# Kernel optimization log

Hardware: AMD Instinct MI355X
Metric: run time of the kernel (lower is better)

Reference implementation:

```python
import jax, jax.numpy as jnp
import numpy as np

NUM_HEAD = 16
EMB_DIM = 1024
HEAD_DIM = EMB_DIM // NUM_HEAD

def setup_inputs() -> dict:
    key = jax.random.key(0)
    ks = jax.random.split(key, 9)
    B, S, D = 2, 2048, EMB_DIM
    s = 1.0 / np.sqrt(D)
    return {
        "x": jax.random.normal(ks[0], (B, S, D), dtype=jnp.float32),
        "Wq": jax.random.normal(ks[1], (D, D), dtype=jnp.float32) * s,
        "bq": jnp.zeros((D,), dtype=jnp.float32),
        "Wk": jax.random.normal(ks[2], (D, D), dtype=jnp.float32) * s,
        "bk": jnp.zeros((D,), dtype=jnp.float32),
        "Wv": jax.random.normal(ks[3], (D, D), dtype=jnp.float32) * s,
        "bv": jnp.zeros((D,), dtype=jnp.float32),
        "Wo": jax.random.normal(ks[4], (D, D), dtype=jnp.float32) * s,
        "bo": jnp.zeros((D,), dtype=jnp.float32),
    }

def reference(x, Wq, bq, Wk, bk, Wv, bv, Wo, bo):
    B, S, D = x.shape
    H, Hd = NUM_HEAD, HEAD_DIM
    # projections (torch Linear: x @ W.T + b; here W stored as [in, out])
    Q = (x @ Wq + bq).reshape(B, S, H, Hd)
    K = (x @ Wk + bk).reshape(B, S, H, Hd)
    V = (x @ Wv + bv).reshape(B, S, H, Hd)
    scale = jnp.sqrt(jnp.asarray(Hd, dtype=x.dtype))
    scores = jnp.einsum('bqhd,bkhd->bhqk', Q, K) / scale  # [B,H,S,S]
    attn = jax.nn.softmax(scores, axis=-1)
    out = jnp.einsum('bhql,blhd->bqhd', attn, V).reshape(B, S, D)
    return out @ Wo + bo
```

## Files before the change

kernel.cpp:

```cpp
#include <hip/hip_runtime.h>
#include <math.h>


using bf16   = __bf16;
using bf16x8 = __attribute__((ext_vector_type(8))) __bf16;
using bf16x4 = __attribute__((ext_vector_type(4))) __bf16;
using f32x4  = __attribute__((ext_vector_type(4))) float;

#define MFMA16(a, b, c) __builtin_amdgcn_mfma_f32_16x16x32_bf16((a), (b), (c), 0, 0, 0)
#define WAIT_VM0() asm volatile("s_waitcnt vmcnt(0)" ::: "memory")

__device__ __forceinline__ bf16x8 ld8(const bf16* p) { return *(const bf16x8*)p; }

__device__ __forceinline__ void ldg_lds16(bf16* lds_base, const bf16* g) {
    __builtin_amdgcn_global_load_lds(
        (const __attribute__((address_space(1))) void*)g,
        (__attribute__((address_space(3))) void*)lds_base, 16, 0, 0);
}

__device__ __forceinline__ float fast_exp2(float x) {
#if __has_builtin(__builtin_amdgcn_exp2f)
    return __builtin_amdgcn_exp2f(x);
#else
    return exp2f(x);
#endif
}

__device__ __forceinline__ float rowsum16(float v) {
    v += __shfl_xor(v, 1, 64);
    v += __shfl_xor(v, 2, 64);
    v += __shfl_xor(v, 4, 64);
    v += __shfl_xor(v, 8, 64);
    return v;
}

__global__ __launch_bounds__(256) void convert_x_kernel(const float* __restrict__ x,
                                                        bf16* __restrict__ xb) {
    int i = (blockIdx.x * 256 + threadIdx.x) * 4;
    float4 v = *(const float4*)&x[i];
    bf16x4 o = { (bf16)v.x, (bf16)v.y, (bf16)v.z, (bf16)v.w };
    *(bf16x4*)&xb[i] = o;
}

__global__ __launch_bounds__(256) void transpose_w_kernel(
    const float* __restrict__ Wq, const float* __restrict__ Wk,
    const float* __restrict__ Wv, const float* __restrict__ Wo,
    bf16* __restrict__ WtBase) {
    __shared__ float tile[32][33];
    const int z = blockIdx.z;
    const float* W = (z == 0) ? Wq : (z == 1) ? Wk : (z == 2) ? Wv : Wo;
    bf16* Wt = WtBase + (size_t)z * 1024 * 1024;
    const int tx = threadIdx.x, ty = threadIdx.y;
    const int x0 = blockIdx.x * 32, y0 = blockIdx.y * 32;
#pragma unroll
    for (int i = 0; i < 4; ++i)
        tile[ty + i * 8][tx] = W[(size_t)(y0 + ty + i * 8) * 1024 + x0 + tx];
    __syncthreads();
#pragma unroll
    for (int i = 0; i < 4; ++i)
        Wt[(size_t)(x0 + ty + i * 8) * 1024 + y0 + tx] = (bf16)tile[tx][ty + i * 8];
}

__device__ __forceinline__ void gemm_stage(const bf16* __restrict__ src, int r0,
                                           int k0, bf16* dst, int w, int lane) {
#pragma unroll
    for (int c = 0; c < 2; ++c) {
        int flat = (w * 2 + c) * 64 + lane;
        int row = flat >> 2, cc = flat & 3;
        int gk = (cc ^ ((row >> 1) & 3)) * 8;
        ldg_lds16(dst + (size_t)(w * 2 + c) * 512,
                  src + (size_t)(r0 + row) * 1024 + k0 + gk);
    }
}

__device__ __forceinline__ void gemm_core_128(const bf16* __restrict__ A,
                                              const bf16* __restrict__ Bt,
                                              int m0, int n0,
                                              bf16* As, bf16* Bs,
                                              f32x4 (&acc)[4][4]) {
    const int tid = threadIdx.x, lane = tid & 63, w = tid >> 6;
    const int lo = lane & 15, quad = lane >> 4;
    const int wm = w >> 1, wn = w & 1;

    gemm_stage(A,  m0, 0, As, w, lane);
    gemm_stage(Bt, n0, 0, Bs, w, lane);
    WAIT_VM0();
    __syncthreads();

    for (int it = 0; it < 32; ++it) {
        const int buf = it & 1;
        if (it + 1 < 32) {
            gemm_stage(A,  m0, (it + 1) * 32, As + (buf ^ 1) * 4096, w, lane);
            gemm_stage(Bt, n0, (it + 1) * 32, Bs + (buf ^ 1) * 4096, w, lane);
        }
        const bf16* Ab = As + buf * 4096;
        const bf16* Bb = Bs + buf * 4096;
        bf16x8 af[4], bq[4];
#pragma unroll
        for (int t = 0; t < 4; ++t) {
            int r = wm * 64 + t * 16 + lo;
            af[t] = ld8(&Ab[r * 32 + ((quad ^ ((r >> 1) & 3)) * 8)]);
        }
#pragma unroll
        for (int t = 0; t < 4; ++t) {
            int r = wn * 64 + t * 16 + lo;
            bq[t] = ld8(&Bb[r * 32 + ((quad ^ ((r >> 1) & 3)) * 8)]);
        }
#pragma unroll
        for (int mt = 0; mt < 4; ++mt)
#pragma unroll
            for (int nt = 0; nt < 4; ++nt)
                acc[mt][nt] = MFMA16(af[mt], bq[nt], acc[mt][nt]);
        WAIT_VM0();
        __syncthreads();
    }
}

__global__ __launch_bounds__(256, 3) void qkv_gemm_kernel(
    const bf16* __restrict__ Xb, const bf16* __restrict__ Wts,
    const float* __restrict__ bq, const float* __restrict__ bk,
    const float* __restrict__ bv,
    bf16* __restrict__ Qo, bf16* __restrict__ Ko, bf16* __restrict__ Vto) {
    __shared__ bf16 Smem[4 * 4096];
    bf16* As = Smem;
    bf16* Bs = Smem + 2 * 4096;
    const int z = blockIdx.z;
    const bf16*  Bt   = Wts + (size_t)z * 1024 * 1024;
    const float* bias = (z == 0) ? bq : (z == 1) ? bk : bv;
    const int m0 = blockIdx.y * 128, n0 = blockIdx.x * 128;

    f32x4 acc[4][4] = {};
    gemm_core_128(Xb, Bt, m0, n0, As, Bs, acc);

    const int tid = threadIdx.x;
    const int lane = tid & 63, w = tid >> 6;
    const int lo = lane & 15, quad = lane >> 4;
    const int wm = w >> 1, wn = w & 1;
    const float QSCALE = 0.125f * 1.44269504088896f;

    if (z == 2) {
        bf16* T = Smem;
        const int b = m0 >> 11;
        const int s_base = m0 & 2047;
#pragma unroll
        for (int half = 0; half < 2; ++half) {
            __syncthreads();
            if (wm == half) {
#pragma unroll
                for (int nt = 0; nt < 4; ++nt)
#pragma unroll
                    for (int mt = 0; mt < 4; ++mt)
#pragma unroll
                        for (int r = 0; r < 4; ++r) {
                            int nn = wn * 64 + nt * 16 + lo;
                            int mm = mt * 16 + quad * 4 + r;
                            T[nn * 68 + mm] = (bf16)(acc[mt][nt][r] + bias[n0 + nn]);
                        }
            }
            __syncthreads();
#pragma unroll
            for (int p = 0; p < 8; ++p) {
                int pos = p * 1024 + tid * 4;
                int row = pos >> 6, col = pos & 63;
                int n = n0 + row, h = n >> 6, hd = n & 63;
                bf16x4 v = *(const bf16x4*)&T[row * 68 + col];
                *(bf16x4*)&Vto[((size_t)((b * 16 + h) * 64 + hd) << 11)
                               + s_base + half * 64 + col] = v;
            }
        }
    } else {
#pragma unroll
        for (int mt = 0; mt < 4; ++mt)
#pragma unroll
            for (int nt = 0; nt < 4; ++nt)
#pragma unroll
                for (int r = 0; r < 4; ++r) {
                    int m = m0 + wm * 64 + mt * 16 + quad * 4 + r;
                    int n = n0 + wn * 64 + nt * 16 + lo;
                    float v = acc[mt][nt][r] + bias[n];
                    int b = m >> 11, s = m & 2047, h = n >> 6, hd = n & 63;
                    if (z == 0)
                        Qo[((size_t)((b * 16 + h) * 2048 + s) << 6) + hd] = (bf16)(v * QSCALE);
                    else
                        Ko[((size_t)((b * 16 + h) * 2048 + s) << 6) + hd] = (bf16)v;
                }
    }
}

__global__ __launch_bounds__(256, 2) void out_gemm_kernel(
    const bf16* __restrict__ A, const bf16* __restrict__ Bt,
    const float* __restrict__ bo, float* __restrict__ Co) {
    __shared__ bf16 As[2 * 2048];
    __shared__ bf16 Bs[2 * 4096];
    const int tid = threadIdx.x, lane = tid & 63, w = tid >> 6;
    const int lo = lane & 15, quad = lane >> 4;
    const int wm = w >> 1, wn = w & 1;
    const int m0 = blockIdx.y * 64, n0 = blockIdx.x * 128;

    auto stageA = [&](int k0, bf16* dst) {
        int flat = w * 64 + lane;
        int row = flat >> 2, cc = flat & 3;
        int gk = (cc ^ ((row >> 1) & 3)) * 8;
        ldg_lds16(dst + (size_t)w * 512, A + (size_t)(m0 + row) * 1024 + k0 + gk);
    };
    auto stageB = [&](int k0, bf16* dst) {
#pragma unroll
        for (int c = 0; c < 2; ++c) {
            int flat = (w * 2 + c) * 64 + lane;
            int row = flat >> 2, cc = flat & 3;
            int gk = (cc ^ ((row >> 1) & 3)) * 8;
            ldg_lds16(dst + (size_t)(w * 2 + c) * 512,
                      Bt + (size_t)(n0 + row) * 1024 + k0 + gk);
        }
    };

    f32x4 acc[2][4] = {};
    stageA(0, As);
    stageB(0, Bs);
    WAIT_VM0();
    __syncthreads();

    for (int it = 0; it < 32; ++it) {
        const int buf = it & 1;
        if (it + 1 < 32) {
            stageA((it + 1) * 32, As + (buf ^ 1) * 2048);
            stageB((it + 1) * 32, Bs + (buf ^ 1) * 4096);
        }
        const bf16* Ab = As + buf * 2048;
        const bf16* Bb = Bs + buf * 4096;
        bf16x8 af[2], bq[4];
#pragma unroll
        for (int t = 0; t < 2; ++t) {
            int r = wm * 32 + t * 16 + lo;
            af[t] = ld8(&Ab[r * 32 + ((quad ^ ((r >> 1) & 3)) * 8)]);
        }
#pragma unroll
        for (int t = 0; t < 4; ++t) {
            int r = wn * 64 + t * 16 + lo;
            bq[t] = ld8(&Bb[r * 32 + ((quad ^ ((r >> 1) & 3)) * 8)]);
        }
#pragma unroll
        for (int mt = 0; mt < 2; ++mt)
#pragma unroll
            for (int nt = 0; nt < 4; ++nt)
                acc[mt][nt] = MFMA16(af[mt], bq[nt], acc[mt][nt]);
        WAIT_VM0();
        __syncthreads();
    }

#pragma unroll
    for (int mt = 0; mt < 2; ++mt)
#pragma unroll
        for (int nt = 0; nt < 4; ++nt)
#pragma unroll
            for (int r = 0; r < 4; ++r) {
                int m = m0 + wm * 32 + mt * 16 + quad * 4 + r;
                int n = n0 + wn * 64 + nt * 16 + lo;
                Co[(size_t)m * 1024 + n] = acc[mt][nt][r] + bo[n];
            }
}

#define PSTRIDE 72

__global__ __launch_bounds__(256, 2) void attn_kernel(
    const bf16* __restrict__ Q, const bf16* __restrict__ K,
    const bf16* __restrict__ Vt, bf16* __restrict__ AO) {
    __shared__ bf16 Ks[2][64 * 64];
    __shared__ bf16 Vs[2][64 * 64];
    __shared__ bf16 Pl[4][32 * PSTRIDE];
    const int tid = threadIdx.x, w = tid >> 6, lane = tid & 63;
    const int lo = lane & 15, quad = lane >> 4;
    const int blk = blockIdx.x;
    const int bh = (blk & 7) | ((blk >> 7) << 3);
    const int qb = (blk >> 3) & 15;
    const int q0 = qb * 128 + w * 32;

    const bf16* Qb = Q + ((size_t)bh * 2048 + q0) * 64;
    const bf16* Kb = K + (size_t)bh * 2048 * 64;
    const bf16* Vb = Vt + (size_t)bh * 64 * 2048;
    bf16* Pw = &Pl[w][0];

    bf16x8 qa[2][2];
#pragma unroll
    for (int mt = 0; mt < 2; ++mt)
#pragma unroll
        for (int ks = 0; ks < 2; ++ks)
            qa[mt][ks] = ld8(&Qb[(mt * 16 + lo) * 64 + ks * 32 + quad * 8]);

    f32x4 O[2][4] = {};
    f32x4 l_acc[2] = {};

    auto stage = [&](int s0, int buf) {
#pragma unroll
        for (int c = 0; c < 2; ++c) {
            int flat = (w * 2 + c) * 64 + lane;
            int row = flat >> 3, cc = flat & 7;
            int gK = (cc ^ ((row >> 2) & 7)) * 8;
            int gV = (cc ^ (row & 7)) * 8;
            ldg_lds16(&Ks[buf][(w * 2 + c) * 512], &Kb[(size_t)(s0 + row) * 64 + gK]);
            ldg_lds16(&Vs[buf][(w * 2 + c) * 512], &Vb[(size_t)row * 2048 + s0 + gV]);
        }
    };

    stage(0, 0);
    WAIT_VM0();
    __syncthreads();

    for (int it = 0; it < 32; ++it) {
        const int buf = it & 1;
        if (it + 1 < 32) stage((it + 1) * 64, buf ^ 1);
        const bf16* Kt = &Ks[buf][0];
        const bf16* Vl = &Vs[buf][0];

        f32x4 S[2][4] = {};
#pragma unroll
        for (int t = 0; t < 4; ++t) {
            int r = lo * 4 + t;
#pragma unroll
            for (int ks = 0; ks < 2; ++ks) {
                bf16x8 kf = ld8(&Kt[r * 64 + (((quad + 4 * ks) ^ ((r >> 2) & 7)) * 8)]);
                S[0][t] = MFMA16(qa[0][ks], kf, S[0][t]);
                S[1][t] = MFMA16(qa[1][ks], kf, S[1][t]);
            }
        }
#pragma unroll
        for (int mt = 0; mt < 2; ++mt)
#pragma unroll
            for (int r = 0; r < 4; ++r) {
                float p0 = fast_exp2(S[mt][0][r]);
                float p1 = fast_exp2(S[mt][1][r]);
                float p2 = fast_exp2(S[mt][2][r]);
                float p3 = fast_exp2(S[mt][3][r]);
                l_acc[mt][r] += (p0 + p1) + (p2 + p3);
                bf16x4 pk = { (bf16)p0, (bf16)p1, (bf16)p2, (bf16)p3 };
                *(bf16x4*)&Pw[(mt * 16 + quad * 4 + r) * PSTRIDE + lo * 4] = pk;
            }
#pragma unroll
        for (int mt = 0; mt < 2; ++mt) {
            bf16x8 pa0 = ld8(&Pw[(mt * 16 + lo) * PSTRIDE + quad * 8]);
            bf16x8 pa1 = ld8(&Pw[(mt * 16 + lo) * PSTRIDE + 32 + quad * 8]);
#pragma unroll
            for (int nt = 0; nt < 4; ++nt) {
                int r = nt * 16 + lo;
                bf16x8 v0 = ld8(&Vl[r * 64 + ((quad ^ (r & 7)) * 8)]);
                bf16x8 v1 = ld8(&Vl[r * 64 + (((quad + 4) ^ (r & 7)) * 8)]);
                O[mt][nt] = MFMA16(pa0, v0, O[mt][nt]);
                O[mt][nt] = MFMA16(pa1, v1, O[mt][nt]);
            }
        }
        WAIT_VM0();
        __syncthreads();
    }

    const int bb = bh >> 4, h = bh & 15;
#pragma unroll
    for (int mt = 0; mt < 2; ++mt) {
        const size_t outbase = ((size_t)(bb * 2048 + q0 + mt * 16)) * 1024 + h * 64;
#pragma unroll
        for (int r = 0; r < 4; ++r) {
            float rl = 1.0f / rowsum16(l_acc[mt][r]);
            size_t rowoff = outbase + (size_t)(quad * 4 + r) * 1024;
#pragma unroll
            for (int nt = 0; nt < 4; ++nt)
                AO[rowoff + nt * 16 + lo] = (bf16)(O[mt][nt][r] * rl);
        }
    }
}

extern "C" void kernel_launch(void* const* d_in, const int* in_sizes, int n_in,
                              void* d_out, int out_size, void* d_ws, size_t ws_size,
                              hipStream_t stream) {
    const float* x  = (const float*)d_in[0];
    const float* Wq = (const float*)d_in[1];
    const float* bq = (const float*)d_in[2];
    const float* Wk = (const float*)d_in[3];
    const float* bk = (const float*)d_in[4];
    const float* Wv = (const float*)d_in[5];
    const float* bv = (const float*)d_in[6];
    const float* Wo = (const float*)d_in[7];
    const float* bo = (const float*)d_in[8];
    float* out = (float*)d_out;

    bf16* wsb = (bf16*)d_ws;
    const size_t M1 = 1024u * 1024u;
    bf16* Xb  = wsb;
    bf16* AO  = wsb;
    bf16* Wt  = wsb + 4 * M1;
    bf16* Qw  = wsb + 8 * M1;
    bf16* Kw  = wsb + 12 * M1;
    bf16* Vtw = wsb + 16 * M1;

    convert_x_kernel<<<4096, 256, 0, stream>>>(x, Xb);
    transpose_w_kernel<<<dim3(32, 32, 4), dim3(32, 8), 0, stream>>>(Wq, Wk, Wv, Wo, Wt);
    qkv_gemm_kernel<<<dim3(8, 32, 3), 256, 0, stream>>>(Xb, Wt, bq, bk, bv, Qw, Kw, Vtw);
    attn_kernel<<<512, 256, 0, stream>>>(Qw, Kw, Vtw, AO);
    out_gemm_kernel<<<dim3(8, 64), 256, 0, stream>>>(AO, Wt + 3 * M1, bo, out);
}
```

Baseline: 191.1 us.

## Deepen attention KV pipeline to 4-stage 32-key tiles and merge prep kernels

The attention kernel now streams K/V in 32-key tiles through a 4-deep LDS ring, issuing loads three tiles ahead. It waits with partial vmcnt counts plus a bare barrier instead of draining all loads every iteration, so global-to-LDS copies overlap compute. The x conversion and weight transpose kernels are merged into one launch to save a kernel launch. The trade-off is twice as many loop iterations and barriers, smaller MFMA batches per iteration, and hand-tuned wait counts that must exactly match the number of outstanding loads.

```diff
diff --git a/kernel.cpp b/kernel.cpp
--- a/kernel.cpp
+++ b/kernel.cpp
@@ -5,10 +5,12 @@
 using bf16   = __bf16;
 using bf16x8 = __attribute__((ext_vector_type(8))) __bf16;
 using bf16x4 = __attribute__((ext_vector_type(4))) __bf16;
+using bf16x2 = __attribute__((ext_vector_type(2))) __bf16;
 using f32x4  = __attribute__((ext_vector_type(4))) float;
 
 #define MFMA16(a, b, c) __builtin_amdgcn_mfma_f32_16x16x32_bf16((a), (b), (c), 0, 0, 0)
 #define WAIT_VM0() asm volatile("s_waitcnt vmcnt(0)" ::: "memory")
+#define WAITBAR(N) asm volatile("s_waitcnt vmcnt(" #N ")\n\ts_barrier" ::: "memory")
 
 __device__ __forceinline__ bf16x8 ld8(const bf16* p) { return *(const bf16x8*)p; }
 
@@ -34,23 +36,28 @@
     return v;
 }
 
-__global__ __launch_bounds__(256) void convert_x_kernel(const float* __restrict__ x,
-                                                        bf16* __restrict__ xb) {
-    int i = (blockIdx.x * 256 + threadIdx.x) * 4;
-    float4 v = *(const float4*)&x[i];
-    bf16x4 o = { (bf16)v.x, (bf16)v.y, (bf16)v.z, (bf16)v.w };
-    *(bf16x4*)&xb[i] = o;
-}
-
-__global__ __launch_bounds__(256) void transpose_w_kernel(
-    const float* __restrict__ Wq, const float* __restrict__ Wk,
-    const float* __restrict__ Wv, const float* __restrict__ Wo,
+__global__ __launch_bounds__(256) void prep_kernel(
+    const float* __restrict__ x, const float* __restrict__ Wq,
+    const float* __restrict__ Wk, const float* __restrict__ Wv,
+    const float* __restrict__ Wo, bf16* __restrict__ xb,
     bf16* __restrict__ WtBase) {
+    const int z = blockIdx.z;
+    const int tid = threadIdx.x;
+    if (z == 4) {
+        int id = blockIdx.y * 32 + blockIdx.x;
+#pragma unroll
+        for (int k = 0; k < 4; ++k) {
+            int i = id * 4096 + k * 1024 + tid * 4;
+            float4 v = *(const float4*)&x[i];
+            bf16x4 o = { (bf16)v.x, (bf16)v.y, (bf16)v.z, (bf16)v.w };
+            *(bf16x4*)&xb[i] = o;
+        }
+        return;
+    }
     __shared__ float tile[32][33];
-    const int z = blockIdx.z;
     const float* W = (z == 0) ? Wq : (z == 1) ? Wk : (z == 2) ? Wv : Wo;
     bf16* Wt = WtBase + (size_t)z * 1024 * 1024;
-    const int tx = threadIdx.x, ty = threadIdx.y;
+    const int tx = tid & 31, ty = tid >> 5;
     const int x0 = blockIdx.x * 32, y0 = blockIdx.y * 32;
 #pragma unroll
     for (int i = 0; i < 4; ++i)
@@ -260,14 +267,14 @@
             }
 }
 
-#define PSTRIDE 72
+#define PSTR 36
 
 __global__ __launch_bounds__(256, 2) void attn_kernel(
     const bf16* __restrict__ Q, const bf16* __restrict__ K,
     const bf16* __restrict__ Vt, bf16* __restrict__ AO) {
-    __shared__ bf16 Ks[2][64 * 64];
-    __shared__ bf16 Vs[2][64 * 64];
-    __shared__ bf16 Pl[4][32 * PSTRIDE];
+    __shared__ bf16 Ks[4][32 * 64];
+    __shared__ bf16 Vs[4][64 * 32];
+    __shared__ bf16 Pl[4][32 * PSTR];
     const int tid = threadIdx.x, w = tid >> 6, lane = tid & 63;
     const int lo = lane & 15, quad = lane >> 4;
     const int blk = blockIdx.x;
@@ -290,35 +297,34 @@
     f32x4 O[2][4] = {};
     f32x4 l_acc[2] = {};
 
+    const int kRow = (w * 64 + lane) >> 3, kCc = lane & 7;
+    const int vRow = (w * 64 + lane) >> 2, vCc = lane & 3;
+    const int gKo = (kCc ^ ((kRow >> 2) & 7)) * 8;
+    const int gVo = (vCc ^ (vRow & 3)) * 8;
     auto stage = [&](int s0, int buf) {
-#pragma unroll
-        for (int c = 0; c < 2; ++c) {
-            int flat = (w * 2 + c) * 64 + lane;
-            int row = flat >> 3, cc = flat & 7;
-            int gK = (cc ^ ((row >> 2) & 7)) * 8;
-            int gV = (cc ^ (row & 7)) * 8;
-            ldg_lds16(&Ks[buf][(w * 2 + c) * 512], &Kb[(size_t)(s0 + row) * 64 + gK]);
-            ldg_lds16(&Vs[buf][(w * 2 + c) * 512], &Vb[(size_t)row * 2048 + s0 + gV]);
-        }
+        ldg_lds16(&Ks[buf][w * 512], &Kb[(size_t)(s0 + kRow) * 64 + gKo]);
+        ldg_lds16(&Vs[buf][w * 512], &Vb[(size_t)vRow * 2048 + s0 + gVo]);
     };
 
     stage(0, 0);
-    WAIT_VM0();
-    __syncthreads();
-
-    for (int it = 0; it < 32; ++it) {
-        const int buf = it & 1;
-        if (it + 1 < 32) stage((it + 1) * 64, buf ^ 1);
+    stage(32, 1);
+    stage(64, 2);
+    WAITBAR(4);
+
+    for (int it = 0; it < 64; ++it) {
+        const int buf = it & 3;
+        if (it + 3 < 64) stage((it + 3) * 32, (it + 3) & 3);
         const bf16* Kt = &Ks[buf][0];
         const bf16* Vl = &Vs[buf][0];
 
-        f32x4 S[2][4] = {};
-#pragma unroll
-        for (int t = 0; t < 4; ++t) {
-            int r = lo * 4 + t;
+        f32x4 S[2][2] = {};
+#pragma unroll
+        for (int t = 0; t < 2; ++t) {
+            int r = lo * 2 + t;
+            int sw = (r >> 2) & 7;
 #pragma unroll
             for (int ks = 0; ks < 2; ++ks) {
-                bf16x8 kf = ld8(&Kt[r * 64 + (((quad + 4 * ks) ^ ((r >> 2) & 7)) * 8)]);
+                bf16x8 kf = ld8(&Kt[r * 64 + (((quad + 4 * ks) ^ sw) * 8)]);
                 S[0][t] = MFMA16(qa[0][ks], kf, S[0][t]);
                 S[1][t] = MFMA16(qa[1][ks], kf, S[1][t]);
             }
@@ -329,27 +335,26 @@
             for (int r = 0; r < 4; ++r) {
                 float p0 = fast_exp2(S[mt][0][r]);
                 float p1 = fast_exp2(S[mt][1][r]);
-                float p2 = fast_exp2(S[mt][2][r]);
-                float p3 = fast_exp2(S[mt][3][r]);
-                l_acc[mt][r] += (p0 + p1) + (p2 + p3);
-                bf16x4 pk = { (bf16)p0, (bf16)p1, (bf16)p2, (bf16)p3 };
-                *(bf16x4*)&Pw[(mt * 16 + quad * 4 + r) * PSTRIDE + lo * 4] = pk;
+                l_acc[mt][r] += p0 + p1;
+                bf16x2 pk = { (bf16)p0, (bf16)p1 };
+                *(bf16x2*)&Pw[(mt * 16 + quad * 4 + r) * PSTR + lo * 2] = pk;
             }
+        bf16x8 vf[4];
+#pragma unroll
+        for (int nt = 0; nt < 4; ++nt) {
+            int r = nt * 16 + lo;
+            vf[nt] = ld8(&Vl[r * 32 + ((quad ^ (r & 3)) * 8)]);
+        }
 #pragma unroll
         for (int mt = 0; mt < 2; ++mt) {
-            bf16x8 pa0 = ld8(&Pw[(mt * 16 + lo) * PSTRIDE + quad * 8]);
-            bf16x8 pa1 = ld8(&Pw[(mt * 16 + lo) * PSTRIDE + 32 + quad * 8]);
-#pragma unroll
-            for (int nt = 0; nt < 4; ++nt) {
-                int r = nt * 16 + lo;
-                bf16x8 v0 = ld8(&Vl[r * 64 + ((quad ^ (r & 7)) * 8)]);
-                bf16x8 v1 = ld8(&Vl[r * 64 + (((quad + 4) ^ (r & 7)) * 8)]);
-                O[mt][nt] = MFMA16(pa0, v0, O[mt][nt]);
-                O[mt][nt] = MFMA16(pa1, v1, O[mt][nt]);
-            }
-        }
-        WAIT_VM0();
-        __syncthreads();
+            bf16x8 pa = ld8(&Pw[(mt * 16 + lo) * PSTR + quad * 8]);
+#pragma unroll
+            for (int nt = 0; nt < 4; ++nt)
+                O[mt][nt] = MFMA16(pa, vf[nt], O[mt][nt]);
+        }
+        if (it < 61)       WAITBAR(4);
+        else if (it == 61) WAITBAR(2);
+        else if (it == 62) WAITBAR(0);
     }
 
     const int bb = bh >> 4, h = bh & 15;
@@ -390,8 +395,7 @@
     bf16* Kw  = wsb + 12 * M1;
     bf16* Vtw = wsb + 16 * M1;
 
-    convert_x_kernel<<<4096, 256, 0, stream>>>(x, Xb);
-    transpose_w_kernel<<<dim3(32, 32, 4), dim3(32, 8), 0, stream>>>(Wq, Wk, Wv, Wo, Wt);
+    prep_kernel<<<dim3(32, 32, 5), 256, 0, stream>>>(x, Wq, Wk, Wv, Wo, Xb, Wt);
     qkv_gemm_kernel<<<dim3(8, 32, 3), 256, 0, stream>>>(Xb, Wt, bq, bk, bv, Qw, Kw, Vtw);
     attn_kernel<<<512, 256, 0, stream>>>(Qw, Kw, Vtw, AO);
     out_gemm_kernel<<<dim3(8, 64), 256, 0, stream>>>(AO, Wt + 3 * M1, bo, out);
```

Result: slower. 213.2 us (+11.5%).

## Triple-buffer LDS pipelines in GEMMs and attention; fuse prep kernels

Applied to the files above, without the earlier changes.

Switches the QKV GEMM, output GEMM and attention K/V staging from double to triple buffering. Loads run two tiles ahead, and the wait keeps the newest tile's loads in flight (vmcnt(N)) with a single barrier per iteration instead of a full drain. The x conversion and weight transposes are merged into one prep launch to cut launch overhead. LDS use per block grows, which may lower occupancy, notably for the qkv GEMM declared with 3 blocks per CU.

```diff
diff --git a/kernel.cpp b/kernel.cpp
--- a/kernel.cpp
+++ b/kernel.cpp
@@ -8,7 +8,7 @@
 using f32x4  = __attribute__((ext_vector_type(4))) float;
 
 #define MFMA16(a, b, c) __builtin_amdgcn_mfma_f32_16x16x32_bf16((a), (b), (c), 0, 0, 0)
-#define WAIT_VM0() asm volatile("s_waitcnt vmcnt(0)" ::: "memory")
+#define WAITBAR(N) asm volatile("s_waitcnt vmcnt(" #N ")\n\ts_barrier" ::: "memory")
 
 __device__ __forceinline__ bf16x8 ld8(const bf16* p) { return *(const bf16x8*)p; }
 
@@ -34,23 +34,28 @@
     return v;
 }
 
-__global__ __launch_bounds__(256) void convert_x_kernel(const float* __restrict__ x,
-                                                        bf16* __restrict__ xb) {
-    int i = (blockIdx.x * 256 + threadIdx.x) * 4;
-    float4 v = *(const float4*)&x[i];
-    bf16x4 o = { (bf16)v.x, (bf16)v.y, (bf16)v.z, (bf16)v.w };
-    *(bf16x4*)&xb[i] = o;
-}
-
-__global__ __launch_bounds__(256) void transpose_w_kernel(
-    const float* __restrict__ Wq, const float* __restrict__ Wk,
-    const float* __restrict__ Wv, const float* __restrict__ Wo,
+__global__ __launch_bounds__(256) void prep_kernel(
+    const float* __restrict__ x, const float* __restrict__ Wq,
+    const float* __restrict__ Wk, const float* __restrict__ Wv,
+    const float* __restrict__ Wo, bf16* __restrict__ xb,
     bf16* __restrict__ WtBase) {
+    const int z = blockIdx.z;
+    const int tid = threadIdx.x;
+    if (z == 4) {
+        int id = blockIdx.y * 32 + blockIdx.x;
+#pragma unroll
+        for (int k = 0; k < 4; ++k) {
+            int i = id * 4096 + k * 1024 + tid * 4;
+            float4 v = *(const float4*)&x[i];
+            bf16x4 o = { (bf16)v.x, (bf16)v.y, (bf16)v.z, (bf16)v.w };
+            *(bf16x4*)&xb[i] = o;
+        }
+        return;
+    }
     __shared__ float tile[32][33];
-    const int z = blockIdx.z;
     const float* W = (z == 0) ? Wq : (z == 1) ? Wk : (z == 2) ? Wv : Wo;
     bf16* Wt = WtBase + (size_t)z * 1024 * 1024;
-    const int tx = threadIdx.x, ty = threadIdx.y;
+    const int tx = tid & 31, ty = tid >> 5;
     const int x0 = blockIdx.x * 32, y0 = blockIdx.y * 32;
 #pragma unroll
     for (int i = 0; i < 4; ++i)
@@ -82,19 +87,9 @@
     const int lo = lane & 15, quad = lane >> 4;
     const int wm = w >> 1, wn = w & 1;
 
-    gemm_stage(A,  m0, 0, As, w, lane);
-    gemm_stage(Bt, n0, 0, Bs, w, lane);
-    WAIT_VM0();
-    __syncthreads();
-
-    for (int it = 0; it < 32; ++it) {
-        const int buf = it & 1;
-        if (it + 1 < 32) {
-            gemm_stage(A,  m0, (it + 1) * 32, As + (buf ^ 1) * 4096, w, lane);
-            gemm_stage(Bt, n0, (it + 1) * 32, Bs + (buf ^ 1) * 4096, w, lane);
-        }
-        const bf16* Ab = As + buf * 4096;
-        const bf16* Bb = Bs + buf * 4096;
+    auto body = [&](int rbuf) {
+        const bf16* Ab = As + rbuf * 4096;
+        const bf16* Bb = Bs + rbuf * 4096;
         bf16x8 af[4], bq[4];
 #pragma unroll
         for (int t = 0; t < 4; ++t) {
@@ -111,9 +106,27 @@
 #pragma unroll
             for (int nt = 0; nt < 4; ++nt)
                 acc[mt][nt] = MFMA16(af[mt], bq[nt], acc[mt][nt]);
-        WAIT_VM0();
-        __syncthreads();
-    }
+    };
+
+    gemm_stage(A,  m0, 0,  As, w, lane);
+    gemm_stage(Bt, n0, 0,  Bs, w, lane);
+    gemm_stage(A,  m0, 32, As + 4096, w, lane);
+    gemm_stage(Bt, n0, 32, Bs + 4096, w, lane);
+    WAITBAR(4);
+
+    int rbuf = 0, sbuf = 2;
+    for (int it = 0; it < 30; ++it) {
+        gemm_stage(A,  m0, (it + 2) * 32, As + sbuf * 4096, w, lane);
+        gemm_stage(Bt, n0, (it + 2) * 32, Bs + sbuf * 4096, w, lane);
+        sbuf = (sbuf == 2) ? 0 : sbuf + 1;
+        body(rbuf);
+        WAITBAR(4);
+        rbuf = (rbuf == 2) ? 0 : rbuf + 1;
+    }
+    body(rbuf);
+    WAITBAR(0);
+    rbuf = (rbuf == 2) ? 0 : rbuf + 1;
+    body(rbuf);
 }
 
 __global__ __launch_bounds__(256, 3) void qkv_gemm_kernel(
@@ -121,9 +134,9 @@
     const float* __restrict__ bq, const float* __restrict__ bk,
     const float* __restrict__ bv,
     bf16* __restrict__ Qo, bf16* __restrict__ Ko, bf16* __restrict__ Vto) {
-    __shared__ bf16 Smem[4 * 4096];
+    __shared__ bf16 Smem[6 * 4096];
     bf16* As = Smem;
-    bf16* Bs = Smem + 2 * 4096;
+    bf16* Bs = Smem + 3 * 4096;
     const int z = blockIdx.z;
     const bf16*  Bt   = Wts + (size_t)z * 1024 * 1024;
     const float* bias = (z == 0) ? bq : (z == 1) ? bk : bv;
@@ -190,44 +203,35 @@
 __global__ __launch_bounds__(256, 2) void out_gemm_kernel(
     const bf16* __restrict__ A, const bf16* __restrict__ Bt,
     const float* __restrict__ bo, float* __restrict__ Co) {
-    __shared__ bf16 As[2 * 2048];
-    __shared__ bf16 Bs[2 * 4096];
+    __shared__ bf16 As[3 * 2048];
+    __shared__ bf16 Bs[3 * 4096];
     const int tid = threadIdx.x, lane = tid & 63, w = tid >> 6;
     const int lo = lane & 15, quad = lane >> 4;
     const int wm = w >> 1, wn = w & 1;
     const int m0 = blockIdx.y * 64, n0 = blockIdx.x * 128;
 
-    auto stageA = [&](int k0, bf16* dst) {
-        int flat = w * 64 + lane;
-        int row = flat >> 2, cc = flat & 3;
-        int gk = (cc ^ ((row >> 1) & 3)) * 8;
-        ldg_lds16(dst + (size_t)w * 512, A + (size_t)(m0 + row) * 1024 + k0 + gk);
-    };
-    auto stageB = [&](int k0, bf16* dst) {
+    auto stage = [&](int k0, int buf) {
+        {
+            int flat = w * 64 + lane;
+            int row = flat >> 2, cc = flat & 3;
+            int gk = (cc ^ ((row >> 1) & 3)) * 8;
+            ldg_lds16(As + buf * 2048 + (size_t)w * 512,
+                      A + (size_t)(m0 + row) * 1024 + k0 + gk);
+        }
 #pragma unroll
         for (int c = 0; c < 2; ++c) {
             int flat = (w * 2 + c) * 64 + lane;
             int row = flat >> 2, cc = flat & 3;
             int gk = (cc ^ ((row >> 1) & 3)) * 8;
-            ldg_lds16(dst + (size_t)(w * 2 + c) * 512,
+            ldg_lds16(Bs + buf * 4096 + (size_t)(w * 2 + c) * 512,
                       Bt + (size_t)(n0 + row) * 1024 + k0 + gk);
         }
     };
 
     f32x4 acc[2][4] = {};
-    stageA(0, As);
-    stageB(0, Bs);
-    WAIT_VM0();
-    __syncthreads();
-
-    for (int it = 0; it < 32; ++it) {
-        const int buf = it & 1;
-        if (it + 1 < 32) {
-            stageA((it + 1) * 32, As + (buf ^ 1) * 2048);
-            stageB((it + 1) * 32, Bs + (buf ^ 1) * 4096);
-        }
-        const bf16* Ab = As + buf * 2048;
-        const bf16* Bb = Bs + buf * 4096;
+    auto body = [&](int rbuf) {
+        const bf16* Ab = As + rbuf * 2048;
+        const bf16* Bb = Bs + rbuf * 4096;
         bf16x8 af[2], bq[4];
 #pragma unroll
         for (int t = 0; t < 2; ++t) {
@@ -244,9 +248,24 @@
 #pragma unroll
             for (int nt = 0; nt < 4; ++nt)
                 acc[mt][nt] = MFMA16(af[mt], bq[nt], acc[mt][nt]);
-        WAIT_VM0();
-        __syncthreads();
-    }
+    };
+
+    stage(0, 0);
+    stage(32, 1);
+    WAITBAR(3);
+
+    int rbuf = 0, sbuf = 2;
+    for (int it = 0; it < 30; ++it) {
+        stage((it + 2) * 32, sbuf);
+        sbuf = (sbuf == 2) ? 0 : sbuf + 1;
+        body(rbuf);
+        WAITBAR(3);
+        rbuf = (rbuf == 2) ? 0 : rbuf + 1;
+    }
+    body(rbuf);
+    WAITBAR(0);
+    rbuf = (rbuf == 2) ? 0 : rbuf + 1;
+    body(rbuf);
 
 #pragma unroll
     for (int mt = 0; mt < 2; ++mt)
@@ -265,8 +284,8 @@
 __global__ __launch_bounds__(256, 2) void attn_kernel(
     const bf16* __restrict__ Q, const bf16* __restrict__ K,
     const bf16* __restrict__ Vt, bf16* __restrict__ AO) {
-    __shared__ bf16 Ks[2][64 * 64];
-    __shared__ bf16 Vs[2][64 * 64];
+    __shared__ bf16 Ks[3][64 * 64];
+    __shared__ bf16 Vs[3][64 * 64];
     __shared__ bf16 Pl[4][32 * PSTRIDE];
     const int tid = threadIdx.x, w = tid >> 6, lane = tid & 63;
     const int lo = lane & 15, quad = lane >> 4;
@@ -302,16 +321,9 @@
         }
     };
 
-    stage(0, 0);
-    WAIT_VM0();
-    __syncthreads();
-
-    for (int it = 0; it < 32; ++it) {
-        const int buf = it & 1;
-        if (it + 1 < 32) stage((it + 1) * 64, buf ^ 1);
-        const bf16* Kt = &Ks[buf][0];
-        const bf16* Vl = &Vs[buf][0];
-
+    auto body = [&](int rbuf) {
+        const bf16* Kt = &Ks[rbuf][0];
+        const bf16* Vl = &Vs[rbuf][0];
         f32x4 S[2][4] = {};
 #pragma unroll
         for (int t = 0; t < 4; ++t) {
@@ -348,9 +360,24 @@
                 O[mt][nt] = MFMA16(pa1, v1, O[mt][nt]);
             }
         }
-        WAIT_VM0();
-        __syncthreads();
-    }
+    };
+
+    stage(0, 0);
+    stage(64, 1);
+    WAITBAR(4);
+
+    int rbuf = 0, sbuf = 2;
+    for (int it = 0; it < 30; ++it) {
+        stage((it + 2) * 64, sbuf);
+        sbuf = (sbuf == 2) ? 0 : sbuf + 1;
+        body(rbuf);
+        WAITBAR(4);
+        rbuf = (rbuf == 2) ? 0 : rbuf + 1;
+    }
+    body(rbuf);
+    WAITBAR(0);
+    rbuf = (rbuf == 2) ? 0 : rbuf + 1;
+    body(rbuf);
 
     const int bb = bh >> 4, h = bh & 15;
 #pragma unroll
@@ -390,8 +417,7 @@
     bf16* Kw  = wsb + 12 * M1;
     bf16* Vtw = wsb + 16 * M1;
 
-    convert_x_kernel<<<4096, 256, 0, stream>>>(x, Xb);
-    transpose_w_kernel<<<dim3(32, 32, 4), dim3(32, 8), 0, stream>>>(Wq, Wk, Wv, Wo, Wt);
+    prep_kernel<<<dim3(32, 32, 5), 256, 0, stream>>>(x, Wq, Wk, Wv, Wo, Xb, Wt);
     qkv_gemm_kernel<<<dim3(8, 32, 3), 256, 0, stream>>>(Xb, Wt, bq, bk, bv, Qw, Kw, Vtw);
     attn_kernel<<<512, 256, 0, stream>>>(Qw, Kw, Vtw, AO);
     out_gemm_kernel<<<dim3(8, 64), 256, 0, stream>>>(AO, Wt + 3 * M1, bo, out);
```

Result: slower. 195.4 us (+2.3%).
